# Optimization experiments

Hardware: AMD Instinct MI355X
Metric: run time of the kernel (lower is better)

The kernel has to match this reference:

```python
import math
import jax, jax.numpy as jnp
import numpy as np

DIM = 1024
B, T = 4, 2048


def setup_inputs() -> dict:
    key = jax.random.key(0)
    ks = jax.random.split(key, 7)
    std = 0.02
    x = jax.random.normal(ks[0], (B, T, DIM), dtype=jnp.float32)
    Wq = jax.random.normal(ks[1], (DIM, DIM), dtype=jnp.float32) * std
    Wk = jax.random.normal(ks[2], (DIM, DIM), dtype=jnp.float32) * std
    Wv = jax.random.normal(ks[3], (DIM, DIM), dtype=jnp.float32) * std
    Wo = jax.random.normal(ks[4], (DIM, DIM), dtype=jnp.float32) * std
    # decay_proj: torch init is zero weight, bias = decay_init; use a small random
    # weight so the data-dependent decay path is exercised.
    Wd = jax.random.normal(ks[5], (1, DIM), dtype=jnp.float32) * std
    bd = jnp.full((1,), 3.0, dtype=jnp.float32)  # decay_init
    out_scale = jnp.full((1,), 0.1, dtype=jnp.float32)
    return {"x": x, "Wq": Wq, "Wk": Wk, "Wv": Wv, "Wo": Wo,
            "Wd": Wd, "bd": bd, "out_scale": out_scale}


def reference(x, Wq, Wk, Wv, Wo, Wd, bd, out_scale):
    Bsz, Tlen, dim = x.shape
    scale = 1.0 / math.sqrt(dim)
    # torch Linear: y = x @ W.T
    q = jnp.einsum('btd,ed->bte', x, Wq)
    k = jnp.einsum('btd,ed->bte', x, Wk)
    v = jnp.einsum('btd,ed->bte', x, Wv)
    scores = jnp.einsum('btd,bsd->bts', q, k) * scale            # [B,T,T]
    decay_logits = jnp.einsum('btd,ed->bte', x, Wd)[..., 0] + bd  # [B,T]
    decay = jax.nn.sigmoid(decay_logits)
    pos = jnp.arange(Tlen)
    diff = pos[None, :] - pos[:, None]                            # diff[i,j] = j - i
    causal = (diff > 0).astype(x.dtype)                           # [T,T]
    log_decay = jnp.log(decay + 1e-8)                             # [B,T]
    dist = jnp.clip(diff.astype(x.dtype) - 1.0, 0.0)              # [T,T]
    # log_weights[b,i,j] = log_decay[b,j] * dist[i,j]
    log_weights = log_decay[:, None, :] * dist[None, :, :]
    weights = jnp.exp(log_weights) * causal[None, :, :]
    scores = scores * weights
    retrieved = jnp.einsum('bts,bsd->btd', scores, v)
    out = jnp.einsum('btd,ed->bte', retrieved, Wo) * out_scale
    return out
```

## Files before the change

### kernel.cpp

```cpp
#include <hip/hip_runtime.h>


using u16 = unsigned short;
typedef __bf16 bf16x8 __attribute__((ext_vector_type(8)));
typedef float f32x4 __attribute__((ext_vector_type(4)));

#define BM 128
#define BN 128
#define BKK 64

__device__ inline u16 f2bf(float f) {
  unsigned u = __builtin_bit_cast(unsigned, f);
  unsigned r = (u + 0x7FFFu + ((u >> 16) & 1u)) >> 16;
  return (u16)r;
}

__device__ inline void gload16(const u16* g, u16* l) {
  __builtin_amdgcn_global_load_lds(
      (const __attribute__((address_space(1))) void*)g,
      (__attribute__((address_space(3))) void*)l, 16, 0, 0);
}

__global__ void cast_f32_bf16(const float* __restrict__ in, u16* __restrict__ out, int n) {
  int i = (blockIdx.x * blockDim.x + threadIdx.x) * 4;
  if (i >= n) return;
  float4 f = *reinterpret_cast<const float4*>(in + i);
  ushort4 o;
  o.x = f2bf(f.x); o.y = f2bf(f.y); o.z = f2bf(f.z); o.w = f2bf(f.w);
  *reinterpret_cast<ushort4*>(out + i) = o;
}

__global__ __launch_bounds__(256) void decay_kernel(const float* __restrict__ x,
    const float* __restrict__ Wd, const float* __restrict__ bd,
    float* __restrict__ ldec) {
  int row = blockIdx.x * 4 + (threadIdx.x >> 6);
  int lane = threadIdx.x & 63;
  const float4* xr = reinterpret_cast<const float4*>(x + (size_t)row * 1024);
  const float4* wd = reinterpret_cast<const float4*>(Wd);
  float s = 0.f;
  #pragma unroll
  for (int i = 0; i < 4; ++i) {
    float4 a = xr[lane + 64 * i];
    float4 b = wd[lane + 64 * i];
    s += a.x * b.x + a.y * b.y + a.z * b.z + a.w * b.w;
  }
  #pragma unroll
  for (int off = 32; off > 0; off >>= 1) s += __shfl_xor(s, off);
  if (lane == 0) {
    float logit = s + bd[0];
    float dec = 1.f / (1.f + expf(-logit));
    ldec[row] = logf(dec + 1e-8f);
  }
}

template <int EPI>
__global__ __launch_bounds__(256, 2)
void gemm_bt(const u16* __restrict__ Ab, const u16* __restrict__ Bb,
             void* __restrict__ Cv, int lda, int ldb, int ldc, int K,
             int tiles_n, int diag, const float* __restrict__ ldec,
             const float* __restrict__ scale_ptr,
             long long abs_, long long bbs_, long long cbs_, int ld_stride) {
  __shared__ __align__(16) u16 lsA[BM * BKK];
  __shared__ __align__(16) u16 lsB[BN * BKK];

  const int batch = blockIdx.y;
  const u16* A = Ab + (size_t)batch * abs_;
  const u16* B = Bb + (size_t)batch * bbs_;

  const int it = blockIdx.x / tiles_n;
  const int jt = blockIdx.x % tiles_n;
  if (EPI == 1 && jt < it) return;
  const int m0 = it * BM, n0 = jt * BN;

  const int tid = threadIdx.x;
  const int lane = tid & 63;
  const int w = tid >> 6;
  const int wm = (w >> 1) * 64, wn = (w & 1) * 64;
  const int l15 = lane & 15, lhi = lane >> 4;

  const int srow = lane >> 3;
  const int schunk = (lane & 7) ^ srow;

  f32x4 acc[4][4];
  #pragma unroll
  for (int i = 0; i < 4; ++i)
    #pragma unroll
    for (int j = 0; j < 4; ++j) acc[i][j] = (f32x4)0.f;

  const int kt0 = diag ? it * (BM / BKK) : 0;
  const int nkt = K / BKK;

  for (int kt = kt0; kt < nkt; ++kt) {
    const int k0 = kt * BKK;
    __syncthreads();
    #pragma unroll
    for (int is = 0; is < 4; ++is) {
      int r = (is * 4 + w) * 8 + srow;
      gload16(A + (size_t)(m0 + r) * lda + (k0 + schunk * 8), &lsA[(is * 4 + w) * 512]);
    }
    #pragma unroll
    for (int is = 0; is < 4; ++is) {
      int r = (is * 4 + w) * 8 + srow;
      gload16(B + (size_t)(n0 + r) * ldb + (k0 + schunk * 8), &lsB[(is * 4 + w) * 512]);
    }
    __syncthreads();
    #pragma unroll
    for (int kk = 0; kk < 2; ++kk) {
      bf16x8 af[4], bv[4];
      #pragma unroll
      for (int mi = 0; mi < 4; ++mi) {
        int r = wm + mi * 16 + l15;
        int s = (kk * 4 + lhi) ^ (r & 7);
        af[mi] = *reinterpret_cast<const bf16x8*>(&lsA[r * 64 + s * 8]);
      }
      #pragma unroll
      for (int ni = 0; ni < 4; ++ni) {
        int r = wn + ni * 16 + l15;
        int s = (kk * 4 + lhi) ^ (r & 7);
        bv[ni] = *reinterpret_cast<const bf16x8*>(&lsB[r * 64 + s * 8]);
      }
      #pragma unroll
      for (int mi = 0; mi < 4; ++mi)
        #pragma unroll
        for (int ni = 0; ni < 4; ++ni)
          acc[mi][ni] = __builtin_amdgcn_mfma_f32_16x16x32_bf16(af[mi], bv[ni], acc[mi][ni], 0, 0, 0);
    }
  }

  if (EPI == 0) {
    u16* C = (u16*)Cv + (size_t)batch * cbs_;
    #pragma unroll
    for (int mi = 0; mi < 4; ++mi)
      #pragma unroll
      for (int q = 0; q < 4; ++q) {
        int row = m0 + wm + mi * 16 + lhi * 4 + q;
        u16* crow = C + (size_t)row * ldc + n0 + wn + l15;
        #pragma unroll
        for (int ni = 0; ni < 4; ++ni) crow[ni * 16] = f2bf(acc[mi][ni][q]);
      }
  } else if (EPI == 1) {
    u16* C = (u16*)Cv + (size_t)batch * cbs_;
    const float* ldb_ = ldec + (size_t)batch * ld_stride;
    float ldv[4];
    #pragma unroll
    for (int ni = 0; ni < 4; ++ni) ldv[ni] = ldb_[n0 + wn + ni * 16 + l15];
    const float sc = 0.03125f;
    #pragma unroll
    for (int mi = 0; mi < 4; ++mi)
      #pragma unroll
      for (int q = 0; q < 4; ++q) {
        int row = m0 + wm + mi * 16 + lhi * 4 + q;
        u16* crow = C + (size_t)row * ldc + n0 + wn + l15;
        #pragma unroll
        for (int ni = 0; ni < 4; ++ni) {
          int col = n0 + wn + ni * 16 + l15;
          int d = col - row;
          float wgt = (d > 0) ? expf(ldv[ni] * (float)(d - 1)) : 0.f;
          crow[ni * 16] = f2bf(acc[mi][ni][q] * sc * wgt);
        }
      }
  } else {
    float* C = (float*)Cv + (size_t)batch * cbs_;
    const float sc = scale_ptr[0];
    #pragma unroll
    for (int mi = 0; mi < 4; ++mi)
      #pragma unroll
      for (int q = 0; q < 4; ++q) {
        int row = m0 + wm + mi * 16 + lhi * 4 + q;
        float* crow = C + (size_t)row * ldc + n0 + wn + l15;
        #pragma unroll
        for (int ni = 0; ni < 4; ++ni) crow[ni * 16] = acc[mi][ni][q] * sc;
      }
  }
}

extern "C" void kernel_launch(void* const* d_in, const int* in_sizes, int n_in,
                              void* d_out, int out_size, void* d_ws, size_t ws_size,
                              hipStream_t stream) {
  const float* x   = (const float*)d_in[0];
  const float* Wq  = (const float*)d_in[1];
  const float* Wk  = (const float*)d_in[2];
  const float* Wv  = (const float*)d_in[3];
  const float* Wo  = (const float*)d_in[4];
  const float* Wd  = (const float*)d_in[5];
  const float* bd  = (const float*)d_in[6];
  const float* osc = (const float*)d_in[7];
  float* out = (float*)d_out;

  char* ws = (char*)d_ws;
  size_t off = 0;
  u16* Xbf = (u16*)(ws + off); off += (size_t)8192 * 1024 * 2;
  u16* Wqk = (u16*)(ws + off); off += (size_t)2048 * 1024 * 2;
  u16* Wvb = (u16*)(ws + off); off += (size_t)1024 * 1024 * 2;
  u16* Wob = (u16*)(ws + off); off += (size_t)1024 * 1024 * 2;
  u16* VT  = (u16*)(ws + off); off += (size_t)1024 * 8192 * 2;
  u16* S   = (u16*)(ws + off); off += (size_t)4 * 2048 * 2048 * 2;
  float* ldec = (float*)(ws + off); off += (size_t)8192 * 4;
  u16* QK  = (u16*)(ws + off); off += (size_t)8192 * 2048 * 2;
  u16* R   = QK;

  cast_f32_bf16<<<8192, 256, 0, stream>>>(x, Xbf, 8192 * 1024);
  cast_f32_bf16<<<1024, 256, 0, stream>>>(Wq, Wqk, 1024 * 1024);
  cast_f32_bf16<<<1024, 256, 0, stream>>>(Wk, Wqk + 1024 * 1024, 1024 * 1024);
  cast_f32_bf16<<<1024, 256, 0, stream>>>(Wv, Wvb, 1024 * 1024);
  cast_f32_bf16<<<1024, 256, 0, stream>>>(Wo, Wob, 1024 * 1024);

  decay_kernel<<<2048, 256, 0, stream>>>(x, Wd, bd, ldec);

  gemm_bt<0><<<dim3(64 * 16, 1), 256, 0, stream>>>(
      Xbf, Wqk, QK, 1024, 1024, 2048, 1024, 16, 0, nullptr, nullptr, 0, 0, 0, 0);

  gemm_bt<0><<<dim3(8 * 64, 1), 256, 0, stream>>>(
      Wvb, Xbf, VT, 1024, 1024, 8192, 1024, 64, 0, nullptr, nullptr, 0, 0, 0, 0);

  gemm_bt<1><<<dim3(16 * 16, 4), 256, 0, stream>>>(
      QK, QK + 1024, S, 2048, 2048, 2048, 1024, 16, 0, ldec, nullptr,
      4194304LL, 4194304LL, 4194304LL, 2048);

  gemm_bt<0><<<dim3(16 * 8, 4), 256, 0, stream>>>(
      S, VT, R, 2048, 8192, 1024, 2048, 8, 1, nullptr, nullptr,
      4194304LL, 2048LL, 2097152LL, 0);

  gemm_bt<2><<<dim3(64 * 8, 1), 256, 0, stream>>>(
      R, Wob, out, 1024, 1024, 1024, 1024, 8, 0, nullptr, osc, 0, 0, 0, 0);
}
```

Before: 185.2 us.

## Add 256x256 pipelined GEMM kernel and fuse cast and decay launches

Introduces a 512-thread GEMM with 256x256 tiles that double-buffers LDS, stages quarter-tiles two k-steps ahead, and interleaves LDS reads, global loads and MFMA with barriers and priority hints. It is used for the QK projection, the scores, the retrieval and the output GEMMs. The x cast is fused with the decay computation, and the four weight casts are merged into one launch. The goal is more data reuse per tile, latency hidden behind MFMA work, and fewer launches, in exchange for far fewer blocks on the smaller GEMMs (e.g. 128 blocks for the output GEMM, 128 for retrieval) and tight hand-scheduled waitcnt logic.

```diff
diff --git a/kernel.cpp b/kernel.cpp
--- a/kernel.cpp
+++ b/kernel.cpp
@@ -4,10 +4,6 @@
 using u16 = unsigned short;
 typedef __bf16 bf16x8 __attribute__((ext_vector_type(8)));
 typedef float f32x4 __attribute__((ext_vector_type(4)));
-
-#define BM 128
-#define BN 128
-#define BKK 64
 
 __device__ inline u16 f2bf(float f) {
   unsigned u = __builtin_bit_cast(unsigned, f);
@@ -21,37 +17,45 @@
       (__attribute__((address_space(3))) void*)l, 16, 0, 0);
 }
 
-__global__ void cast_f32_bf16(const float* __restrict__ in, u16* __restrict__ out, int n) {
-  int i = (blockIdx.x * blockDim.x + threadIdx.x) * 4;
-  if (i >= n) return;
-  float4 f = *reinterpret_cast<const float4*>(in + i);
+__global__ __launch_bounds__(256) void xcast_decay(const float* __restrict__ x,
+    u16* __restrict__ Xbf, const float* __restrict__ Wd,
+    const float* __restrict__ bd, float* __restrict__ ldec) {
+  int row = blockIdx.x;
+  int t = threadIdx.x;
+  float4 f = reinterpret_cast<const float4*>(x + (size_t)row * 1024)[t];
+  float4 g = reinterpret_cast<const float4*>(Wd)[t];
   ushort4 o;
   o.x = f2bf(f.x); o.y = f2bf(f.y); o.z = f2bf(f.z); o.w = f2bf(f.w);
-  *reinterpret_cast<ushort4*>(out + i) = o;
-}
-
-__global__ __launch_bounds__(256) void decay_kernel(const float* __restrict__ x,
-    const float* __restrict__ Wd, const float* __restrict__ bd,
-    float* __restrict__ ldec) {
-  int row = blockIdx.x * 4 + (threadIdx.x >> 6);
-  int lane = threadIdx.x & 63;
-  const float4* xr = reinterpret_cast<const float4*>(x + (size_t)row * 1024);
-  const float4* wd = reinterpret_cast<const float4*>(Wd);
-  float s = 0.f;
-  #pragma unroll
-  for (int i = 0; i < 4; ++i) {
-    float4 a = xr[lane + 64 * i];
-    float4 b = wd[lane + 64 * i];
-    s += a.x * b.x + a.y * b.y + a.z * b.z + a.w * b.w;
-  }
+  reinterpret_cast<ushort4*>(Xbf + (size_t)row * 1024)[t] = o;
+  float s = f.x * g.x + f.y * g.y + f.z * g.z + f.w * g.w;
   #pragma unroll
   for (int off = 32; off > 0; off >>= 1) s += __shfl_xor(s, off);
-  if (lane == 0) {
-    float logit = s + bd[0];
-    float dec = 1.f / (1.f + expf(-logit));
+  __shared__ float red[4];
+  if ((t & 63) == 0) red[t >> 6] = s;
+  __syncthreads();
+  if (t == 0) {
+    float tot = red[0] + red[1] + red[2] + red[3];
+    float dec = 1.f / (1.f + expf(-(tot + bd[0])));
     ldec[row] = logf(dec + 1e-8f);
   }
 }
+
+__global__ __launch_bounds__(256) void wcast(const float* __restrict__ Wq,
+    const float* __restrict__ Wk, const float* __restrict__ Wv,
+    const float* __restrict__ Wo, u16* __restrict__ Wall) {
+  int b = blockIdx.x;
+  int m = b >> 10;
+  const float* src = (m == 0) ? Wq : (m == 1) ? Wk : (m == 2) ? Wv : Wo;
+  int i = ((b & 1023) * 256 + threadIdx.x) * 4;
+  float4 f = *reinterpret_cast<const float4*>(src + i);
+  ushort4 o;
+  o.x = f2bf(f.x); o.y = f2bf(f.y); o.z = f2bf(f.z); o.w = f2bf(f.w);
+  *reinterpret_cast<ushort4*>(Wall + (size_t)m * 1048576 + i) = o;
+}
+
+#define BM 128
+#define BN 128
+#define BKK 64
 
 template <int EPI>
 __global__ __launch_bounds__(256, 2)
@@ -77,7 +81,6 @@
   const int w = tid >> 6;
   const int wm = (w >> 1) * 64, wn = (w & 1) * 64;
   const int l15 = lane & 15, lhi = lane >> 4;
-
   const int srow = lane >> 3;
   const int schunk = (lane & 7) ^ srow;
 
@@ -172,6 +175,202 @@
         for (int ni = 0; ni < 4; ++ni) crow[ni * 16] = acc[mi][ni][q] * sc;
       }
   }
+}
+
+
+#define SBAR0() __builtin_amdgcn_sched_barrier(0)
+
+template <int EPI>
+__global__ __launch_bounds__(512, 2)
+void gemm256(const u16* __restrict__ Ab, const u16* __restrict__ Bb,
+             void* __restrict__ Cv, int lda, int ldb, int ldc, int K,
+             int tiles_n, int diag, const float* __restrict__ ldec,
+             const float* __restrict__ scale_ptr,
+             long long abs_, long long bbs_, long long cbs_, int ld_stride) {
+  __shared__ __align__(16) u16 lds2[65536];
+
+  const int batch = blockIdx.y;
+  const u16* A = Ab + (size_t)batch * abs_;
+  const u16* B = Bb + (size_t)batch * bbs_;
+
+  const int it = blockIdx.x / tiles_n;
+  const int jt = blockIdx.x % tiles_n;
+  if (EPI == 1 && jt < it) return;
+  const int m0 = it * 256, n0 = jt * 256;
+
+  const int tid = threadIdx.x;
+  const int lane = tid & 63;
+  const int w = tid >> 6;
+  const int wm = w >> 2, wn = w & 3;
+  const int l15 = lane & 15, lhi = lane >> 4;
+  const int lr8 = lane >> 3;
+  const int schunk = (lane & 7) ^ lr8;
+
+  const int kt0 = diag ? it * 4 : 0;
+  const int nkt = K / 64;
+  const int span = nkt - kt0;
+
+  f32x4 acc[8][4];
+  #pragma unroll
+  for (int i = 0; i < 8; ++i)
+    #pragma unroll
+    for (int j = 0; j < 4; ++j) acc[i][j] = (f32x4)0.f;
+
+  auto stageA = [&](int qm, int kt, int buf) {
+    #pragma unroll
+    for (int li = 0; li < 2; ++li) {
+      int u = li * 8 + w;
+      int h = u >> 3;
+      int rl = qm * 64 + (u & 7) * 8;
+      gload16(A + (size_t)(m0 + h * 128 + rl + lr8) * lda + (size_t)(kt * 64 + schunk * 8),
+              &lds2[buf * 32768 + h * 8192 + rl * 64]);
+    }
+  };
+  auto stageB = [&](int qn, int kt, int buf) {
+    #pragma unroll
+    for (int li = 0; li < 2; ++li) {
+      int u = li * 8 + w;
+      int h = u >> 3, sub = (u >> 2) & 1;
+      int rl = qn * 32 + sub * 64 + (u & 3) * 8;
+      gload16(B + (size_t)(n0 + h * 128 + rl + lr8) * ldb + (size_t)(kt * 64 + schunk * 8),
+              &lds2[buf * 32768 + 16384 + h * 8192 + rl * 64]);
+    }
+  };
+
+  bf16x8 af[4][2], bv[2][2];
+  auto readA = [&](int qm, int buf) {
+    const u16* base = &lds2[buf * 32768 + wm * 8192];
+    #pragma unroll
+    for (int mi = 0; mi < 4; ++mi) {
+      int r = qm * 64 + mi * 16 + l15;
+      #pragma unroll
+      for (int kk = 0; kk < 2; ++kk) {
+        int s = (kk * 4 + lhi) ^ (r & 7);
+        af[mi][kk] = *reinterpret_cast<const bf16x8*>(&base[r * 64 + s * 8]);
+      }
+    }
+  };
+  auto readB = [&](int qn, int buf) {
+    const u16* base = &lds2[buf * 32768 + 16384 + (wn >> 1) * 8192];
+    #pragma unroll
+    for (int ni = 0; ni < 2; ++ni) {
+      int r = (wn & 1) * 64 + qn * 32 + ni * 16 + l15;
+      #pragma unroll
+      for (int kk = 0; kk < 2; ++kk) {
+        int s = (kk * 4 + lhi) ^ (r & 7);
+        bv[ni][kk] = *reinterpret_cast<const bf16x8*>(&base[r * 64 + s * 8]);
+      }
+    }
+  };
+  auto mmaq = [&](int qm, int qn) {
+    #pragma unroll
+    for (int kk = 0; kk < 2; ++kk)
+      #pragma unroll
+      for (int mi = 0; mi < 4; ++mi)
+        #pragma unroll
+        for (int ni = 0; ni < 2; ++ni)
+          acc[qm * 4 + mi][qn * 2 + ni] = __builtin_amdgcn_mfma_f32_16x16x32_bf16(
+              af[mi][kk], bv[ni][kk], acc[qm * 4 + mi][qn * 2 + ni], 0, 0, 0);
+  };
+
+  {
+    int k0 = kt0;
+    int k1 = kt0 + (1 < span ? 1 : 0);
+    stageA(0, k0, 0); stageB(0, k0, 0); stageA(1, k0, 0); stageB(1, k0, 0);
+    stageA(0, k1, 1); stageB(1, k1, 1); stageA(1, k1, 1);
+  }
+  asm volatile("s_waitcnt vmcnt(6)" ::: "memory");
+  __builtin_amdgcn_s_barrier();
+  SBAR0();
+
+  for (int t = 0; t < span; ++t) {
+    const int buf = t & 1, nb = buf ^ 1;
+    int t1 = t + 1; if (t1 >= span) t1 -= span;
+    int t2 = t + 2; if (t2 >= span) t2 -= span;
+    const int kt1 = kt0 + t1, kt2 = kt0 + t2;
+
+    readA(0, buf); readB(0, buf);
+    stageB(0, kt1, nb);
+    SBAR0(); __builtin_amdgcn_s_barrier();
+    asm volatile("s_waitcnt lgkmcnt(0)" ::: "memory"); SBAR0();
+    __builtin_amdgcn_s_setprio(1); mmaq(0, 0); __builtin_amdgcn_s_setprio(0);
+    SBAR0(); __builtin_amdgcn_s_barrier(); SBAR0();
+
+    readB(1, buf);
+    stageA(0, kt2, buf);
+    SBAR0(); __builtin_amdgcn_s_barrier();
+    asm volatile("s_waitcnt lgkmcnt(0)" ::: "memory"); SBAR0();
+    __builtin_amdgcn_s_setprio(1); mmaq(0, 1); __builtin_amdgcn_s_setprio(0);
+    SBAR0(); __builtin_amdgcn_s_barrier(); SBAR0();
+
+    readA(1, buf);
+    stageB(1, kt2, buf);
+    SBAR0(); __builtin_amdgcn_s_barrier();
+    asm volatile("s_waitcnt lgkmcnt(0)" ::: "memory"); SBAR0();
+    __builtin_amdgcn_s_setprio(1); mmaq(1, 1); __builtin_amdgcn_s_setprio(0);
+    SBAR0(); __builtin_amdgcn_s_barrier(); SBAR0();
+
+    readB(0, buf);
+    stageA(1, kt2, buf);
+    SBAR0(); __builtin_amdgcn_s_barrier();
+    asm volatile("s_waitcnt lgkmcnt(0)" ::: "memory"); SBAR0();
+    __builtin_amdgcn_s_setprio(1); mmaq(1, 0); __builtin_amdgcn_s_setprio(0);
+    asm volatile("s_waitcnt vmcnt(6)" ::: "memory");
+    SBAR0(); __builtin_amdgcn_s_barrier(); SBAR0();
+  }
+
+  if (EPI == 0) {
+    u16* C = (u16*)Cv + (size_t)batch * cbs_;
+    #pragma unroll
+    for (int a = 0; a < 8; ++a) {
+      int ro = (a >> 2) * 64 + (a & 3) * 16;
+      #pragma unroll
+      for (int q = 0; q < 4; ++q) {
+        int row = m0 + wm * 128 + ro + lhi * 4 + q;
+        u16* crow = C + (size_t)row * ldc + n0 + wn * 64 + l15;
+        #pragma unroll
+        for (int ni = 0; ni < 4; ++ni) crow[ni * 16] = f2bf(acc[a][ni][q]);
+      }
+    }
+  } else if (EPI == 1) {
+    u16* C = (u16*)Cv + (size_t)batch * cbs_;
+    const float* ldp = ldec + (size_t)batch * ld_stride;
+    float ldv[4];
+    #pragma unroll
+    for (int ni = 0; ni < 4; ++ni) ldv[ni] = ldp[n0 + wn * 64 + ni * 16 + l15];
+    const float sc = 0.03125f;
+    #pragma unroll
+    for (int a = 0; a < 8; ++a) {
+      int ro = (a >> 2) * 64 + (a & 3) * 16;
+      #pragma unroll
+      for (int q = 0; q < 4; ++q) {
+        int row = m0 + wm * 128 + ro + lhi * 4 + q;
+        u16* crow = C + (size_t)row * ldc + n0 + wn * 64 + l15;
+        #pragma unroll
+        for (int ni = 0; ni < 4; ++ni) {
+          int col = n0 + wn * 64 + ni * 16 + l15;
+          int d = col - row;
+          float wgt = (d > 0) ? expf(ldv[ni] * (float)(d - 1)) : 0.f;
+          crow[ni * 16] = f2bf(acc[a][ni][q] * sc * wgt);
+        }
+      }
+    }
+  } else {
+    float* C = (float*)Cv + (size_t)batch * cbs_;
+    const float sc = scale_ptr[0];
+    #pragma unroll
+    for (int a = 0; a < 8; ++a) {
+      int ro = (a >> 2) * 64 + (a & 3) * 16;
+      #pragma unroll
+      for (int q = 0; q < 4; ++q) {
+        int row = m0 + wm * 128 + ro + lhi * 4 + q;
+        float* crow = C + (size_t)row * ldc + n0 + wn * 64 + l15;
+        #pragma unroll
+        for (int ni = 0; ni < 4; ++ni) crow[ni * 16] = acc[a][ni][q] * sc;
+      }
+    }
+  }
+  asm volatile("s_waitcnt vmcnt(0)" ::: "memory");
 }
 
 extern "C" void kernel_launch(void* const* d_in, const int* in_sizes, int n_in,
@@ -189,38 +388,35 @@
 
   char* ws = (char*)d_ws;
   size_t off = 0;
-  u16* Xbf = (u16*)(ws + off); off += (size_t)8192 * 1024 * 2;
-  u16* Wqk = (u16*)(ws + off); off += (size_t)2048 * 1024 * 2;
-  u16* Wvb = (u16*)(ws + off); off += (size_t)1024 * 1024 * 2;
-  u16* Wob = (u16*)(ws + off); off += (size_t)1024 * 1024 * 2;
-  u16* VT  = (u16*)(ws + off); off += (size_t)1024 * 8192 * 2;
-  u16* S   = (u16*)(ws + off); off += (size_t)4 * 2048 * 2048 * 2;
+  u16* Xbf  = (u16*)(ws + off); off += (size_t)8192 * 1024 * 2;
+  u16* Wall = (u16*)(ws + off); off += (size_t)4096 * 1024 * 2;
+  u16* VT   = (u16*)(ws + off); off += (size_t)1024 * 8192 * 2;
+  u16* S    = (u16*)(ws + off); off += (size_t)4 * 2048 * 2048 * 2;
   float* ldec = (float*)(ws + off); off += (size_t)8192 * 4;
-  u16* QK  = (u16*)(ws + off); off += (size_t)8192 * 2048 * 2;
-  u16* R   = QK;
-
-  cast_f32_bf16<<<8192, 256, 0, stream>>>(x, Xbf, 8192 * 1024);
-  cast_f32_bf16<<<1024, 256, 0, stream>>>(Wq, Wqk, 1024 * 1024);
-  cast_f32_bf16<<<1024, 256, 0, stream>>>(Wk, Wqk + 1024 * 1024, 1024 * 1024);
-  cast_f32_bf16<<<1024, 256, 0, stream>>>(Wv, Wvb, 1024 * 1024);
-  cast_f32_bf16<<<1024, 256, 0, stream>>>(Wo, Wob, 1024 * 1024);
-
-  decay_kernel<<<2048, 256, 0, stream>>>(x, Wd, bd, ldec);
-
-  gemm_bt<0><<<dim3(64 * 16, 1), 256, 0, stream>>>(
-      Xbf, Wqk, QK, 1024, 1024, 2048, 1024, 16, 0, nullptr, nullptr, 0, 0, 0, 0);
+  u16* QK   = (u16*)(ws + off); off += (size_t)8192 * 2048 * 2;
+  u16* R    = QK;
+
+  u16* Wqk = Wall;
+  u16* Wvb = Wall + 2 * 1048576;
+  u16* Wob = Wall + 3 * 1048576;
+
+  xcast_decay<<<8192, 256, 0, stream>>>(x, Xbf, Wd, bd, ldec);
+  wcast<<<4096, 256, 0, stream>>>(Wq, Wk, Wv, Wo, Wall);
+
+  gemm256<0><<<dim3(32 * 8, 1), 512, 0, stream>>>(
+      Xbf, Wqk, QK, 1024, 1024, 2048, 1024, 8, 0, nullptr, nullptr, 0, 0, 0, 0);
 
   gemm_bt<0><<<dim3(8 * 64, 1), 256, 0, stream>>>(
       Wvb, Xbf, VT, 1024, 1024, 8192, 1024, 64, 0, nullptr, nullptr, 0, 0, 0, 0);
 
-  gemm_bt<1><<<dim3(16 * 16, 4), 256, 0, stream>>>(
-      QK, QK + 1024, S, 2048, 2048, 2048, 1024, 16, 0, ldec, nullptr,
+  gemm256<1><<<dim3(8 * 8, 4), 512, 0, stream>>>(
+      QK, QK + 1024, S, 2048, 2048, 2048, 1024, 8, 0, ldec, nullptr,
       4194304LL, 4194304LL, 4194304LL, 2048);
 
-  gemm_bt<0><<<dim3(16 * 8, 4), 256, 0, stream>>>(
-      S, VT, R, 2048, 8192, 1024, 2048, 8, 1, nullptr, nullptr,
+  gemm256<0><<<dim3(8 * 4, 4), 512, 0, stream>>>(
+      S, VT, R, 2048, 8192, 1024, 2048, 4, 1, nullptr, nullptr,
       4194304LL, 2048LL, 2097152LL, 0);
 
-  gemm_bt<2><<<dim3(64 * 8, 1), 256, 0, stream>>>(
-      R, Wob, out, 1024, 1024, 1024, 1024, 8, 0, nullptr, osc, 0, 0, 0, 0);
-}
+  gemm256<2><<<dim3(32 * 4, 1), 512, 0, stream>>>(
+      R, Wob, out, 1024, 1024, 1024, 1024, 4, 0, nullptr, osc, 0, 0, 0, 0);
+}
```

After: 216.7 us. 17.0% more time.

## Triple-buffer GEMM with 256x128 tiles, fuse cast and decay kernels

Applied to the files above, without the earlier changes.

Rewrites the shared GEMM as a 512-thread, 256x128-tile kernel with a three-stage LDS ring. Loads for tile t+2 are issued while MFMAs run on tile t, and the per-k-step double __syncthreads is replaced by vmcnt waits and a single barrier. The x cast is fused with the decay projection, and the four weight casts are merged into one launch to cut launch count and re-reading of x. In exchange it uses much more LDS per block (144 KB), which limits occupancy, and the larger tiles waste more work on the causal diagonal.

```diff
diff --git a/kernel.cpp b/kernel.cpp
--- a/kernel.cpp
+++ b/kernel.cpp
@@ -4,10 +4,6 @@
 using u16 = unsigned short;
 typedef __bf16 bf16x8 __attribute__((ext_vector_type(8)));
 typedef float f32x4 __attribute__((ext_vector_type(4)));
-
-#define BM 128
-#define BN 128
-#define BKK 64
 
 __device__ inline u16 f2bf(float f) {
   unsigned u = __builtin_bit_cast(unsigned, f);
@@ -21,47 +17,50 @@
       (__attribute__((address_space(3))) void*)l, 16, 0, 0);
 }
 
-__global__ void cast_f32_bf16(const float* __restrict__ in, u16* __restrict__ out, int n) {
-  int i = (blockIdx.x * blockDim.x + threadIdx.x) * 4;
-  if (i >= n) return;
-  float4 f = *reinterpret_cast<const float4*>(in + i);
+__global__ __launch_bounds__(256) void xcast_decay(const float* __restrict__ x,
+    u16* __restrict__ Xbf, const float* __restrict__ Wd,
+    const float* __restrict__ bd, float* __restrict__ ldec) {
+  int row = blockIdx.x;
+  int t = threadIdx.x;
+  float4 f = reinterpret_cast<const float4*>(x + (size_t)row * 1024)[t];
+  float4 g = reinterpret_cast<const float4*>(Wd)[t];
   ushort4 o;
   o.x = f2bf(f.x); o.y = f2bf(f.y); o.z = f2bf(f.z); o.w = f2bf(f.w);
-  *reinterpret_cast<ushort4*>(out + i) = o;
-}
-
-__global__ __launch_bounds__(256) void decay_kernel(const float* __restrict__ x,
-    const float* __restrict__ Wd, const float* __restrict__ bd,
-    float* __restrict__ ldec) {
-  int row = blockIdx.x * 4 + (threadIdx.x >> 6);
-  int lane = threadIdx.x & 63;
-  const float4* xr = reinterpret_cast<const float4*>(x + (size_t)row * 1024);
-  const float4* wd = reinterpret_cast<const float4*>(Wd);
-  float s = 0.f;
-  #pragma unroll
-  for (int i = 0; i < 4; ++i) {
-    float4 a = xr[lane + 64 * i];
-    float4 b = wd[lane + 64 * i];
-    s += a.x * b.x + a.y * b.y + a.z * b.z + a.w * b.w;
-  }
+  reinterpret_cast<ushort4*>(Xbf + (size_t)row * 1024)[t] = o;
+  float s = f.x * g.x + f.y * g.y + f.z * g.z + f.w * g.w;
   #pragma unroll
   for (int off = 32; off > 0; off >>= 1) s += __shfl_xor(s, off);
-  if (lane == 0) {
-    float logit = s + bd[0];
-    float dec = 1.f / (1.f + expf(-logit));
+  __shared__ float red[4];
+  if ((t & 63) == 0) red[t >> 6] = s;
+  __syncthreads();
+  if (t == 0) {
+    float tot = red[0] + red[1] + red[2] + red[3];
+    float dec = 1.f / (1.f + expf(-(tot + bd[0])));
     ldec[row] = logf(dec + 1e-8f);
   }
 }
 
+__global__ __launch_bounds__(256) void wcast(const float* __restrict__ Wq,
+    const float* __restrict__ Wk, const float* __restrict__ Wv,
+    const float* __restrict__ Wo, u16* __restrict__ Wall) {
+  int b = blockIdx.x;
+  int m = b >> 10;
+  const float* src = (m == 0) ? Wq : (m == 1) ? Wk : (m == 2) ? Wv : Wo;
+  int i = ((b & 1023) * 256 + threadIdx.x) * 4;
+  float4 f = *reinterpret_cast<const float4*>(src + i);
+  ushort4 o;
+  o.x = f2bf(f.x); o.y = f2bf(f.y); o.z = f2bf(f.z); o.w = f2bf(f.w);
+  *reinterpret_cast<ushort4*>(Wall + (size_t)m * 1048576 + i) = o;
+}
+
 template <int EPI>
-__global__ __launch_bounds__(256, 2)
-void gemm_bt(const u16* __restrict__ Ab, const u16* __restrict__ Bb,
-             void* __restrict__ Cv, int lda, int ldb, int ldc, int K,
-             int tiles_n, int diag, const float* __restrict__ ldec,
-             const float* __restrict__ scale_ptr,
-             long long abs_, long long bbs_, long long cbs_, int ld_stride) {
-  __shared__ __align__(16) u16 lsA[BM * BKK];
-  __shared__ __align__(16) u16 lsB[BN * BKK];
+__global__ __launch_bounds__(512, 2)
+void gemm3(const u16* __restrict__ Ab, const u16* __restrict__ Bb,
+           void* __restrict__ Cv, int lda, int ldb, int ldc, int K,
+           int tiles_n, int diag, const float* __restrict__ ldec,
+           const float* __restrict__ scale_ptr,
+           long long abs_, long long bbs_, long long cbs_, int ld_stride) {
+  __shared__ __align__(16) u16 lds2[73728];
 
   const int batch = blockIdx.y;
   const u16* A = Ab + (size_t)batch * abs_;
@@ -69,17 +68,20 @@
 
   const int it = blockIdx.x / tiles_n;
   const int jt = blockIdx.x % tiles_n;
-  if (EPI == 1 && jt < it) return;
-  const int m0 = it * BM, n0 = jt * BN;
+  if (EPI == 1 && jt < 2 * it) return;
+  const int m0 = it * 256, n0 = jt * 128;
 
   const int tid = threadIdx.x;
   const int lane = tid & 63;
   const int w = tid >> 6;
-  const int wm = (w >> 1) * 64, wn = (w & 1) * 64;
+  const int wm = w >> 1, wn = w & 1;
   const int l15 = lane & 15, lhi = lane >> 4;
-
-  const int srow = lane >> 3;
-  const int schunk = (lane & 7) ^ srow;
+  const int lr8 = lane >> 3;
+  const int schunk = (lane & 7) ^ lr8;
+
+  const int kt0 = diag ? it * 4 : 0;
+  const int nkt = K / 64;
+  const int span = nkt - kt0;
 
   f32x4 acc[4][4];
   #pragma unroll
@@ -87,45 +89,70 @@
     #pragma unroll
     for (int j = 0; j < 4; ++j) acc[i][j] = (f32x4)0.f;
 
-  const int kt0 = diag ? it * (BM / BKK) : 0;
-  const int nkt = K / BKK;
-
-  for (int kt = kt0; kt < nkt; ++kt) {
-    const int k0 = kt * BKK;
-    __syncthreads();
-    #pragma unroll
-    for (int is = 0; is < 4; ++is) {
-      int r = (is * 4 + w) * 8 + srow;
-      gload16(A + (size_t)(m0 + r) * lda + (k0 + schunk * 8), &lsA[(is * 4 + w) * 512]);
+  auto stage = [&](int kt, int buf) {
+    const size_t kb = (size_t)kt * 64 + schunk * 8;
+    u16* lb = &lds2[buf * 24576];
+    #pragma unroll
+    for (int u = 0; u < 4; ++u)
+      gload16(A + (size_t)(m0 + u * 64 + w * 8 + lr8) * lda + kb,
+              lb + (u * 64 + w * 8) * 64);
+    #pragma unroll
+    for (int u = 0; u < 2; ++u)
+      gload16(B + (size_t)(n0 + u * 64 + w * 8 + lr8) * ldb + kb,
+              lb + 16384 + (u * 64 + w * 8) * 64);
+  };
+
+  stage(kt0, 0);
+  stage(kt0 + 1, 1);
+  asm volatile("s_waitcnt vmcnt(6)" ::: "memory");
+  __builtin_amdgcn_s_barrier();
+
+  int bR = 0, bS = 2;
+  for (int t = 0; t < span; ++t) {
+    const u16* baseA = &lds2[bR * 24576];
+    const u16* baseB = baseA + 16384;
+
+    bf16x8 af[4][2], bv[4][2];
+    #pragma unroll
+    for (int mi = 0; mi < 4; ++mi) {
+      int r = wm * 64 + mi * 16 + l15;
+      #pragma unroll
+      for (int kk = 0; kk < 2; ++kk) {
+        int s = (kk * 4 + lhi) ^ (r & 7);
+        af[mi][kk] = *reinterpret_cast<const bf16x8*>(&baseA[r * 64 + s * 8]);
+      }
     }
     #pragma unroll
-    for (int is = 0; is < 4; ++is) {
-      int r = (is * 4 + w) * 8 + srow;
-      gload16(B + (size_t)(n0 + r) * ldb + (k0 + schunk * 8), &lsB[(is * 4 + w) * 512]);
+    for (int ni = 0; ni < 4; ++ni) {
+      int r = wn * 64 + ni * 16 + l15;
+      #pragma unroll
+      for (int kk = 0; kk < 2; ++kk) {
+        int s = (kk * 4 + lhi) ^ (r & 7);
+        bv[ni][kk] = *reinterpret_cast<const bf16x8*>(&baseB[r * 64 + s * 8]);
+      }
     }
-    __syncthreads();
-    #pragma unroll
-    for (int kk = 0; kk < 2; ++kk) {
-      bf16x8 af[4], bv[4];
-      #pragma unroll
-      for (int mi = 0; mi < 4; ++mi) {
-        int r = wm + mi * 16 + l15;
-        int s = (kk * 4 + lhi) ^ (r & 7);
-        af[mi] = *reinterpret_cast<const bf16x8*>(&lsA[r * 64 + s * 8]);
-      }
-      #pragma unroll
-      for (int ni = 0; ni < 4; ++ni) {
-        int r = wn + ni * 16 + l15;
-        int s = (kk * 4 + lhi) ^ (r & 7);
-        bv[ni] = *reinterpret_cast<const bf16x8*>(&lsB[r * 64 + s * 8]);
-      }
+
+    int t2 = t + 2; if (t2 >= span) t2 = span - 1;
+    stage(kt0 + t2, bS);
+
+    __builtin_amdgcn_s_setprio(1);
+    #pragma unroll
+    for (int kk = 0; kk < 2; ++kk)
       #pragma unroll
       for (int mi = 0; mi < 4; ++mi)
         #pragma unroll
         for (int ni = 0; ni < 4; ++ni)
-          acc[mi][ni] = __builtin_amdgcn_mfma_f32_16x16x32_bf16(af[mi], bv[ni], acc[mi][ni], 0, 0, 0);
-    }
+          acc[mi][ni] = __builtin_amdgcn_mfma_f32_16x16x32_bf16(
+              af[mi][kk], bv[ni][kk], acc[mi][ni], 0, 0, 0);
+    __builtin_amdgcn_s_setprio(0);
+
+    asm volatile("s_waitcnt vmcnt(6)" ::: "memory");
+    __builtin_amdgcn_s_barrier();
+
+    bR = (bR == 2) ? 0 : bR + 1;
+    bS = (bS == 2) ? 0 : bS + 1;
   }
+  asm volatile("s_waitcnt vmcnt(0)" ::: "memory");
 
   if (EPI == 0) {
     u16* C = (u16*)Cv + (size_t)batch * cbs_;
@@ -133,27 +160,27 @@
     for (int mi = 0; mi < 4; ++mi)
       #pragma unroll
       for (int q = 0; q < 4; ++q) {
-        int row = m0 + wm + mi * 16 + lhi * 4 + q;
-        u16* crow = C + (size_t)row * ldc + n0 + wn + l15;
+        int row = m0 + wm * 64 + mi * 16 + lhi * 4 + q;
+        u16* crow = C + (size_t)row * ldc + n0 + wn * 64 + l15;
         #pragma unroll
         for (int ni = 0; ni < 4; ++ni) crow[ni * 16] = f2bf(acc[mi][ni][q]);
       }
   } else if (EPI == 1) {
     u16* C = (u16*)Cv + (size_t)batch * cbs_;
-    const float* ldb_ = ldec + (size_t)batch * ld_stride;
+    const float* ldp = ldec + (size_t)batch * ld_stride;
     float ldv[4];
     #pragma unroll
-    for (int ni = 0; ni < 4; ++ni) ldv[ni] = ldb_[n0 + wn + ni * 16 + l15];
+    for (int ni = 0; ni < 4; ++ni) ldv[ni] = ldp[n0 + wn * 64 + ni * 16 + l15];
     const float sc = 0.03125f;
     #pragma unroll
     for (int mi = 0; mi < 4; ++mi)
       #pragma unroll
       for (int q = 0; q < 4; ++q) {
-        int row = m0 + wm + mi * 16 + lhi * 4 + q;
-        u16* crow = C + (size_t)row * ldc + n0 + wn + l15;
+        int row = m0 + wm * 64 + mi * 16 + lhi * 4 + q;
+        u16* crow = C + (size_t)row * ldc + n0 + wn * 64 + l15;
         #pragma unroll
         for (int ni = 0; ni < 4; ++ni) {
-          int col = n0 + wn + ni * 16 + l15;
+          int col = n0 + wn * 64 + ni * 16 + l15;
           int d = col - row;
           float wgt = (d > 0) ? expf(ldv[ni] * (float)(d - 1)) : 0.f;
           crow[ni * 16] = f2bf(acc[mi][ni][q] * sc * wgt);
@@ -166,8 +193,8 @@
     for (int mi = 0; mi < 4; ++mi)
       #pragma unroll
       for (int q = 0; q < 4; ++q) {
-        int row = m0 + wm + mi * 16 + lhi * 4 + q;
-        float* crow = C + (size_t)row * ldc + n0 + wn + l15;
+        int row = m0 + wm * 64 + mi * 16 + lhi * 4 + q;
+        float* crow = C + (size_t)row * ldc + n0 + wn * 64 + l15;
         #pragma unroll
         for (int ni = 0; ni < 4; ++ni) crow[ni * 16] = acc[mi][ni][q] * sc;
       }
@@ -189,38 +216,35 @@
 
   char* ws = (char*)d_ws;
   size_t off = 0;
-  u16* Xbf = (u16*)(ws + off); off += (size_t)8192 * 1024 * 2;
-  u16* Wqk = (u16*)(ws + off); off += (size_t)2048 * 1024 * 2;
-  u16* Wvb = (u16*)(ws + off); off += (size_t)1024 * 1024 * 2;
-  u16* Wob = (u16*)(ws + off); off += (size_t)1024 * 1024 * 2;
-  u16* VT  = (u16*)(ws + off); off += (size_t)1024 * 8192 * 2;
-  u16* S   = (u16*)(ws + off); off += (size_t)4 * 2048 * 2048 * 2;
+  u16* Xbf  = (u16*)(ws + off); off += (size_t)8192 * 1024 * 2;
+  u16* Wall = (u16*)(ws + off); off += (size_t)4096 * 1024 * 2;
+  u16* VT   = (u16*)(ws + off); off += (size_t)1024 * 8192 * 2;
+  u16* S    = (u16*)(ws + off); off += (size_t)4 * 2048 * 2048 * 2;
   float* ldec = (float*)(ws + off); off += (size_t)8192 * 4;
-  u16* QK  = (u16*)(ws + off); off += (size_t)8192 * 2048 * 2;
-  u16* R   = QK;
-
-  cast_f32_bf16<<<8192, 256, 0, stream>>>(x, Xbf, 8192 * 1024);
-  cast_f32_bf16<<<1024, 256, 0, stream>>>(Wq, Wqk, 1024 * 1024);
-  cast_f32_bf16<<<1024, 256, 0, stream>>>(Wk, Wqk + 1024 * 1024, 1024 * 1024);
-  cast_f32_bf16<<<1024, 256, 0, stream>>>(Wv, Wvb, 1024 * 1024);
-  cast_f32_bf16<<<1024, 256, 0, stream>>>(Wo, Wob, 1024 * 1024);
-
-  decay_kernel<<<2048, 256, 0, stream>>>(x, Wd, bd, ldec);
-
-  gemm_bt<0><<<dim3(64 * 16, 1), 256, 0, stream>>>(
+  u16* QK   = (u16*)(ws + off); off += (size_t)8192 * 2048 * 2;
+  u16* R    = QK;
+
+  u16* Wqk = Wall;
+  u16* Wvb = Wall + 2 * 1048576;
+  u16* Wob = Wall + 3 * 1048576;
+
+  xcast_decay<<<8192, 256, 0, stream>>>(x, Xbf, Wd, bd, ldec);
+  wcast<<<4096, 256, 0, stream>>>(Wq, Wk, Wv, Wo, Wall);
+
+  gemm3<0><<<dim3(32 * 16, 1), 512, 0, stream>>>(
       Xbf, Wqk, QK, 1024, 1024, 2048, 1024, 16, 0, nullptr, nullptr, 0, 0, 0, 0);
 
-  gemm_bt<0><<<dim3(8 * 64, 1), 256, 0, stream>>>(
+  gemm3<0><<<dim3(4 * 64, 1), 512, 0, stream>>>(
       Wvb, Xbf, VT, 1024, 1024, 8192, 1024, 64, 0, nullptr, nullptr, 0, 0, 0, 0);
 
-  gemm_bt<1><<<dim3(16 * 16, 4), 256, 0, stream>>>(
+  gemm3<1><<<dim3(8 * 16, 4), 512, 0, stream>>>(
       QK, QK + 1024, S, 2048, 2048, 2048, 1024, 16, 0, ldec, nullptr,
       4194304LL, 4194304LL, 4194304LL, 2048);
 
-  gemm_bt<0><<<dim3(16 * 8, 4), 256, 0, stream>>>(
+  gemm3<0><<<dim3(8 * 8, 4), 512, 0, stream>>>(
       S, VT, R, 2048, 8192, 1024, 2048, 8, 1, nullptr, nullptr,
       4194304LL, 2048LL, 2097152LL, 0);
 
-  gemm_bt<2><<<dim3(64 * 8, 1), 256, 0, stream>>>(
+  gemm3<2><<<dim3(32 * 8, 1), 512, 0, stream>>>(
       R, Wob, out, 1024, 1024, 1024, 1024, 8, 0, nullptr, osc, 0, 0, 0, 0);
 }
```

New measurement: 177.3 us. 1.04x faster.
